# Kernel optimization log

Measured on AMD Instinct MI355X. Metric: run time of the kernel, lower is better.

The kernel has to match this reference:

```python
import jax, jax.numpy as jnp
import numpy as np


def setup_inputs() -> dict:
    key = jax.random.key(0)
    k1, k2, k3, k4 = jax.random.split(key, 4)
    B, N, F, H, C = 16, 4096, 8, 64, 256
    x = jax.random.normal(k1, (B, N, F, H), dtype=jnp.float32)
    W = jax.random.normal(k2, (H, 1), dtype=jnp.float32) / jnp.sqrt(jnp.float32(H))
    b = jax.random.normal(k3, (1,), dtype=jnp.float32) * 0.01
    segment_ids = jax.random.randint(k4, (N,), 0, C)
    return {"x": x, "W": W, "b": b, "segment_ids": segment_ids, "num_coarse": C}


def reference(x, W, b, segment_ids, num_coarse):
    # x: [B, N, F, H]; segment_ids: [N] -> coarse index; output: [B, C, F, H]
    B, N, Fdim, H = x.shape
    seg = segment_ids
    # node scores: Linear(hidden_dim, 1) on mean over feature axis -> [B, N]
    scores = (jnp.einsum('bnfh,ho->bn', x, W) / jnp.float32(Fdim)) + b[0]
    # numerically-stable per-segment softmax over fine nodes within each coarse group
    seg_max = jax.vmap(lambda s: jax.ops.segment_max(s, seg, num_segments=num_coarse))(scores)  # [B, C]
    e = jnp.exp(scores - seg_max[:, seg])                                                        # [B, N]
    denom = jax.vmap(lambda ee: jax.ops.segment_sum(ee, seg, num_segments=num_coarse))(e)        # [B, C]
    w = e / denom[:, seg]                                                                        # [B, N]
    # score-weighted segmented sum of fine features into coarse nodes
    pooled = jax.vmap(
        lambda wb, xb: jax.ops.segment_sum(wb[:, None, None] * xb, seg, num_segments=num_coarse)
    )(w, x)  # [B, C, F, H]
    return pooled
```

## Files before the change

kernel.cpp:

```cpp
#include <hip/hip_runtime.h>

#define B_ 16
#define N_ 4096
#define F_ 8
#define H_ 64
#define C_ 256
#define FH 512
#define CAP 256

__global__ __launch_bounds__(256) void fused_pool_kernel(
    const float* __restrict__ x, const float* __restrict__ W,
    const float* __restrict__ bias, const int* __restrict__ seg,
    float* __restrict__ out)
{
    int c    = blockIdx.x & (C_ - 1);
    int g    = blockIdx.x >> 8;
    int t    = threadIdx.x;
    int wave = t >> 6;
    int lane = t & 63;
    int b    = g * 4 + wave;

    __shared__ int list[CAP];
    __shared__ int cnt;
    if (t == 0) cnt = 0;
    __syncthreads();

    const int4* seg4 = (const int4*)seg;
#pragma unroll
    for (int k = 0; k < N_ / (256 * 4); k++) {
        int i4 = t + k * 256;
        int4 s4 = seg4[i4];
        int n0 = i4 * 4;
        if (s4.x == c) { int p = atomicAdd(&cnt, 1); if (p < CAP) list[p] = n0; }
        if (s4.y == c) { int p = atomicAdd(&cnt, 1); if (p < CAP) list[p] = n0 + 1; }
        if (s4.z == c) { int p = atomicAdd(&cnt, 1); if (p < CAP) list[p] = n0 + 2; }
        if (s4.w == c) { int p = atomicAdd(&cnt, 1); if (p < CAP) list[p] = n0 + 3; }
    }
    __syncthreads();
    int m = cnt;
    if (m > CAP) m = CAP;

    float4 w4 = *(const float4*)(W + ((4 * lane) & 63));
    float  bb = bias[0];

    const float4* x4 = (const float4*)x;
    size_t batch_base = (size_t)b * N_ * (FH / 4);

    float4 accA0 = {0, 0, 0, 0}, accA1 = {0, 0, 0, 0};
    float4 accB0 = {0, 0, 0, 0}, accB1 = {0, 0, 0, 0};
    float  esum = 0.0f;

    int i = 0;
    for (; i + 2 <= m; i += 2) {
        int na = list[i], nb = list[i + 1];
        size_t ra = batch_base + (size_t)na * (FH / 4);
        size_t rb = batch_base + (size_t)nb * (FH / 4);
        float4 a0 = x4[ra + lane];
        float4 a1 = x4[ra + 64 + lane];
        float4 b0 = x4[rb + lane];
        float4 b1 = x4[rb + 64 + lane];

        float pa = (a0.x + a1.x) * w4.x + (a0.y + a1.y) * w4.y
                 + (a0.z + a1.z) * w4.z + (a0.w + a1.w) * w4.w;
        float pb = (b0.x + b1.x) * w4.x + (b0.y + b1.y) * w4.y
                 + (b0.z + b1.z) * w4.z + (b0.w + b1.w) * w4.w;
#pragma unroll
        for (int off = 32; off > 0; off >>= 1) {
            pa += __shfl_xor(pa, off, 64);
            pb += __shfl_xor(pb, off, 64);
        }
        float ea = __expf(pa * (1.0f / F_) + bb);
        float eb = __expf(pb * (1.0f / F_) + bb);
        esum += ea + eb;
        accA0.x += ea * a0.x; accA0.y += ea * a0.y; accA0.z += ea * a0.z; accA0.w += ea * a0.w;
        accA1.x += ea * a1.x; accA1.y += ea * a1.y; accA1.z += ea * a1.z; accA1.w += ea * a1.w;
        accB0.x += eb * b0.x; accB0.y += eb * b0.y; accB0.z += eb * b0.z; accB0.w += eb * b0.w;
        accB1.x += eb * b1.x; accB1.y += eb * b1.y; accB1.z += eb * b1.z; accB1.w += eb * b1.w;
    }
    if (i < m) {
        int na = list[i];
        size_t ra = batch_base + (size_t)na * (FH / 4);
        float4 a0 = x4[ra + lane];
        float4 a1 = x4[ra + 64 + lane];
        float pa = (a0.x + a1.x) * w4.x + (a0.y + a1.y) * w4.y
                 + (a0.z + a1.z) * w4.z + (a0.w + a1.w) * w4.w;
#pragma unroll
        for (int off = 32; off > 0; off >>= 1)
            pa += __shfl_xor(pa, off, 64);
        float ea = __expf(pa * (1.0f / F_) + bb);
        esum += ea;
        accA0.x += ea * a0.x; accA0.y += ea * a0.y; accA0.z += ea * a0.z; accA0.w += ea * a0.w;
        accA1.x += ea * a1.x; accA1.y += ea * a1.y; accA1.z += ea * a1.z; accA1.w += ea * a1.w;
    }

    float inv = (m > 0) ? 1.0f / esum : 0.0f;
    float4 r0, r1;
    r0.x = (accA0.x + accB0.x) * inv; r0.y = (accA0.y + accB0.y) * inv;
    r0.z = (accA0.z + accB0.z) * inv; r0.w = (accA0.w + accB0.w) * inv;
    r1.x = (accA1.x + accB1.x) * inv; r1.y = (accA1.y + accB1.y) * inv;
    r1.z = (accA1.z + accB1.z) * inv; r1.w = (accA1.w + accB1.w) * inv;
    size_t ob = ((size_t)(b * C_ + c)) * (FH / 4);
    ((float4*)out)[ob + lane]      = r0;
    ((float4*)out)[ob + 64 + lane] = r1;
}

extern "C" void kernel_launch(void* const* d_in, const int* in_sizes, int n_in,
                              void* d_out, int out_size, void* d_ws, size_t ws_size,
                              hipStream_t stream)
{
    const float* x    = (const float*)d_in[0];
    const float* W    = (const float*)d_in[1];
    const float* bias = (const float*)d_in[2];
    const int*   seg  = (const int*)d_in[3];
    float* out = (float*)d_out;

    fused_pool_kernel<<<C_ * (B_ / 4), 256, 0, stream>>>(x, W, bias, seg, out);
}
```

Before: 207.1 us.

## Split each segment's node list across four waves, one batch per block

Each block now handles a single (batch, coarse segment) pair. Its four waves process interleaved nodes from the segment list, and their partial accumulators and exp sums are reduced through shared memory at the end. The grid grows fourfold, which spreads the per-segment gather across more waves and should raise memory-level parallelism. In exchange, every block rescans segment_ids, so that scan now runs four times as often, and a shared-memory reduction and barrier are added. A launch-bounds occupancy hint is also introduced.

```diff
diff --git a/kernel.cpp b/kernel.cpp
--- a/kernel.cpp
+++ b/kernel.cpp
@@ -8,20 +8,22 @@
 #define FH 512
 #define CAP 256
 
-__global__ __launch_bounds__(256) void fused_pool_kernel(
+__global__ __launch_bounds__(256, 6) void fused_pool_kernel(
     const float* __restrict__ x, const float* __restrict__ W,
     const float* __restrict__ bias, const int* __restrict__ seg,
     float* __restrict__ out)
 {
     int c    = blockIdx.x & (C_ - 1);
-    int g    = blockIdx.x >> 8;
+    int b    = blockIdx.x >> 8;
     int t    = threadIdx.x;
     int wave = t >> 6;
     int lane = t & 63;
-    int b    = g * 4 + wave;
 
-    __shared__ int list[CAP];
-    __shared__ int cnt;
+    __shared__ int    list[CAP];
+    __shared__ int    cnt;
+    __shared__ float4 acc_sh[4][128];
+    __shared__ float  es_sh[4];
+
     if (t == 0) cnt = 0;
     __syncthreads();
 
@@ -46,13 +48,12 @@
     const float4* x4 = (const float4*)x;
     size_t batch_base = (size_t)b * N_ * (FH / 4);
 
-    float4 accA0 = {0, 0, 0, 0}, accA1 = {0, 0, 0, 0};
-    float4 accB0 = {0, 0, 0, 0}, accB1 = {0, 0, 0, 0};
+    float4 acc0 = {0, 0, 0, 0}, acc1 = {0, 0, 0, 0};
     float  esum = 0.0f;
 
-    int i = 0;
-    for (; i + 2 <= m; i += 2) {
-        int na = list[i], nb = list[i + 1];
+    int j = wave;
+    for (; j + 4 < m; j += 8) {
+        int na = list[j], nb = list[j + 4];
         size_t ra = batch_base + (size_t)na * (FH / 4);
         size_t rb = batch_base + (size_t)nb * (FH / 4);
         float4 a0 = x4[ra + lane];
@@ -72,13 +73,13 @@
         float ea = __expf(pa * (1.0f / F_) + bb);
         float eb = __expf(pb * (1.0f / F_) + bb);
         esum += ea + eb;
-        accA0.x += ea * a0.x; accA0.y += ea * a0.y; accA0.z += ea * a0.z; accA0.w += ea * a0.w;
-        accA1.x += ea * a1.x; accA1.y += ea * a1.y; accA1.z += ea * a1.z; accA1.w += ea * a1.w;
-        accB0.x += eb * b0.x; accB0.y += eb * b0.y; accB0.z += eb * b0.z; accB0.w += eb * b0.w;
-        accB1.x += eb * b1.x; accB1.y += eb * b1.y; accB1.z += eb * b1.z; accB1.w += eb * b1.w;
+        acc0.x += ea * a0.x + eb * b0.x; acc0.y += ea * a0.y + eb * b0.y;
+        acc0.z += ea * a0.z + eb * b0.z; acc0.w += ea * a0.w + eb * b0.w;
+        acc1.x += ea * a1.x + eb * b1.x; acc1.y += ea * a1.y + eb * b1.y;
+        acc1.z += ea * a1.z + eb * b1.z; acc1.w += ea * a1.w + eb * b1.w;
     }
-    if (i < m) {
-        int na = list[i];
+    if (j < m) {
+        int na = list[j];
         size_t ra = batch_base + (size_t)na * (FH / 4);
         float4 a0 = x4[ra + lane];
         float4 a1 = x4[ra + 64 + lane];
@@ -89,19 +90,30 @@
             pa += __shfl_xor(pa, off, 64);
         float ea = __expf(pa * (1.0f / F_) + bb);
         esum += ea;
-        accA0.x += ea * a0.x; accA0.y += ea * a0.y; accA0.z += ea * a0.z; accA0.w += ea * a0.w;
-        accA1.x += ea * a1.x; accA1.y += ea * a1.y; accA1.z += ea * a1.z; accA1.w += ea * a1.w;
+        acc0.x += ea * a0.x; acc0.y += ea * a0.y; acc0.z += ea * a0.z; acc0.w += ea * a0.w;
+        acc1.x += ea * a1.x; acc1.y += ea * a1.y; acc1.z += ea * a1.z; acc1.w += ea * a1.w;
     }
 
-    float inv = (m > 0) ? 1.0f / esum : 0.0f;
-    float4 r0, r1;
-    r0.x = (accA0.x + accB0.x) * inv; r0.y = (accA0.y + accB0.y) * inv;
-    r0.z = (accA0.z + accB0.z) * inv; r0.w = (accA0.w + accB0.w) * inv;
-    r1.x = (accA1.x + accB1.x) * inv; r1.y = (accA1.y + accB1.y) * inv;
-    r1.z = (accA1.z + accB1.z) * inv; r1.w = (accA1.w + accB1.w) * inv;
-    size_t ob = ((size_t)(b * C_ + c)) * (FH / 4);
-    ((float4*)out)[ob + lane]      = r0;
-    ((float4*)out)[ob + 64 + lane] = r1;
+    acc_sh[wave][lane]      = acc0;
+    acc_sh[wave][64 + lane] = acc1;
+    if (lane == 0) es_sh[wave] = esum;
+    __syncthreads();
+
+    if (t < 128) {
+        float es  = es_sh[0] + es_sh[1] + es_sh[2] + es_sh[3];
+        float inv = (m > 0) ? 1.0f / es : 0.0f;
+        float4 s0 = acc_sh[0][t];
+        float4 s1 = acc_sh[1][t];
+        float4 s2 = acc_sh[2][t];
+        float4 s3 = acc_sh[3][t];
+        float4 r;
+        r.x = (s0.x + s1.x + s2.x + s3.x) * inv;
+        r.y = (s0.y + s1.y + s2.y + s3.y) * inv;
+        r.z = (s0.z + s1.z + s2.z + s3.z) * inv;
+        r.w = (s0.w + s1.w + s2.w + s3.w) * inv;
+        size_t ob = ((size_t)(b * C_ + c)) * (FH / 4);
+        ((float4*)out)[ob + t] = r;
+    }
 }
 
 extern "C" void kernel_launch(void* const* d_in, const int* in_sizes, int n_in,
@@ -114,5 +126,5 @@
     const int*   seg  = (const int*)d_in[3];
     float* out = (float*)d_out;
 
-    fused_pool_kernel<<<C_ * (B_ / 4), 256, 0, stream>>>(x, W, bias, seg, out);
+    fused_pool_kernel<<<B_ * C_, 256, 0, stream>>>(x, W, bias, seg, out);
 }
```

New measurement: 200.7 us. 1.03x faster.
